# Optimization experiments

Hardware: AMD Instinct MI355X
Metric: run time of the kernel (lower is better)

The kernel has to match this reference:

```python
import jax, jax.numpy as jnp
import numpy as np

B, SEQ_LEN, IN_DIM = 16, 1024, 768
R = 0.1
PI = 3.1415926


def conv1d(x, w, b):
    # x: [B,C,L], w: [O,I,3], 'same' padding, stride 1
    y = jax.lax.conv_general_dilated(x, w, window_strides=(1,), padding=[(1, 1)],
                                     dimension_numbers=('NCH', 'OIH', 'NCH'))
    return y + b[None, :, None]


def layernorm_cl(x, g, b, eps=1e-5):
    # torch nn.LayerNorm((C, L)): normalize jointly over the last two dims of [B,C,L]
    m = x.mean(axis=(1, 2), keepdims=True)
    v = x.var(axis=(1, 2), keepdims=True)
    return (x - m) / jnp.sqrt(v + eps) * g[None] + b[None]


def setup_inputs() -> dict:
    key = jax.random.key(0)
    ks = jax.random.split(key, 8)
    D, D2, L = IN_DIM, IN_DIM * 2, SEQ_LEN
    sc1 = 1.0 / np.sqrt(D * 3)
    sc2 = 1.0 / np.sqrt(D2 * 3)
    return {
        'feats': jax.random.normal(ks[0], (B, L, D), dtype=jnp.float32),
        'conv1_w': jax.random.normal(ks[1], (D2, D, 3), dtype=jnp.float32) * sc1,
        'conv1_b': jnp.zeros((D2,), jnp.float32),
        'ln1_w': jnp.ones((D2, L), jnp.float32),
        'ln1_b': jnp.zeros((D2, L), jnp.float32),
        'conv2_w': jax.random.normal(ks[2], (D2, D2, 3), dtype=jnp.float32) * sc2,
        'conv2_b': jnp.zeros((D2,), jnp.float32),
        'ln2_w': jnp.ones((D2, L), jnp.float32),
        'ln2_b': jnp.zeros((D2, L), jnp.float32),
        'conv3_w': jax.random.normal(ks[3], (2, D2, 3), dtype=jnp.float32) * sc2,
        'conv3_b': jnp.zeros((2,), jnp.float32),
        'ln3_w': jnp.ones((2, L), jnp.float32),
        'ln3_b': jnp.zeros((2, L), jnp.float32),
    }


def reference(feats, conv1_w, conv1_b, ln1_w, ln1_b, conv2_w, conv2_b, ln2_w, ln2_b,
              conv3_w, conv3_b, ln3_w, ln3_b):
    # NOTE: original uses nn.LeakyReLU(True) -> negative_slope=1.0, i.e. identity.
    x = jnp.transpose(feats, (0, 2, 1))                 # [B,D,L]
    h = layernorm_cl(conv1d(x, conv1_w, conv1_b), ln1_w, ln1_b)
    h = layernorm_cl(conv1d(h, conv2_w, conv2_b), ln2_w, ln2_b)
    h = layernorm_cl(conv1d(h, conv3_w, conv3_b), ln3_w, ln3_b)  # [B,2,L]
    s = jax.nn.softmax(h[:, 0, :], axis=1)              # [B,L]
    w = jax.nn.softmax(h[:, 1, :], axis=1)              # [B,L]
    # Vectorized over all centers i: std[b,i] = R*L*s[b,i]
    std = R * SEQ_LEN * s                               # [B,L]
    pos = jnp.arange(SEQ_LEN, dtype=feats.dtype)
    diff2 = (pos[None, :] - pos[:, None]) ** 2          # [i_center, j]
    c = (2.0 * PI) ** -0.5
    gauss = c / std[:, :, None] * jnp.exp(-diff2[None] / (1e-05 + 2.0 * std[:, :, None] ** 2))
    gauss = gauss / jnp.max(gauss, axis=2, keepdims=True)
    att = gauss * w[:, None, :]                         # [B,L_center,L]
    out = jnp.einsum('bij,bjd->bid', att, feats)        # [B,L,D]
    return out
```

## Files before the change

### kernel.cpp

```cpp
#include <hip/hip_runtime.h>
#include <hip/hip_bf16.h>
#include <cstdint>

#define B_   16
#define L_   1024
#define D_   768
#define D2_  1536

typedef __attribute__((ext_vector_type(8))) short bf16x8;
typedef __attribute__((ext_vector_type(4))) float f32x4;

__device__ __forceinline__ float ldin(const void* p, size_t i, int bf) {
  if (bf) return __bfloat162float(((const __hip_bfloat16*)p)[i]);
  return ((const float*)p)[i];
}
__device__ __forceinline__ unsigned short f2bs(float f) {
  __hip_bfloat16 h = __float2bfloat16(f);
  return *(unsigned short*)&h;
}
__device__ __forceinline__ float bs2f(unsigned short u) {
  __hip_bfloat16 h; *(unsigned short*)&h = u;
  return __bfloat162float(h);
}

__device__ __forceinline__ void gload16(const unsigned short* g, unsigned short* l) {
  __builtin_amdgcn_global_load_lds(
      (const __attribute__((address_space(1))) unsigned int*)g,
      (__attribute__((address_space(3))) unsigned int*)l, 16, 0, 0);
}

__global__ void k_detect(const void* __restrict__ ln1w, int* __restrict__ flag) {
  if (threadIdx.x == 0) {
    unsigned u = *(const unsigned*)ln1w;
    *flag = (u == 0x3F800000u) ? 0 : 1;
  }
}

__global__ __launch_bounds__(256) void k_cvt_x(const void* __restrict__ in,
                                               unsigned short* __restrict__ out,
                                               const int* __restrict__ flag) {
  const int bf = *flag;
  const size_t total = (size_t)B_ * (L_ + 2) * D_;
  for (size_t i = (size_t)blockIdx.x * 256 + threadIdx.x; i < total; i += (size_t)gridDim.x * 256) {
    size_t b = i / ((L_ + 2) * D_);
    size_t rem = i - b * (L_ + 2) * D_;
    int pr = (int)(rem / D_);
    int ci = (int)(rem - (size_t)pr * D_);
    float v = 0.f;
    if (pr >= 1 && pr <= L_) v = ldin(in, (b * L_ + pr - 1) * D_ + ci, bf);
    out[i] = f2bs(v);
  }
}

template<int IC>
__global__ __launch_bounds__(256) void k_cvt_w(const void* __restrict__ w,
                                               unsigned short* __restrict__ wp,
                                               const int* __restrict__ flag) {
  const int bf = *flag;
  const int n = D2_ * 3 * IC;
  for (int e = blockIdx.x * 256 + threadIdx.x; e < n; e += gridDim.x * 256) {
    int o = e / (3 * IC); int rem = e - o * 3 * IC;
    int t = rem / IC;     int ci = rem - t * IC;
    wp[e] = f2bs(ldin(w, ((size_t)o * IC + ci) * 3 + t, bf));
  }
}

__global__ __launch_bounds__(256) void k_cvt_lnp(const void* __restrict__ src,
                                                 unsigned short* __restrict__ dst,
                                                 const int* __restrict__ flag) {
  const int bf = *flag;
  __shared__ float t[32][33];
  const int l0 = blockIdx.x * 32, c0 = blockIdx.y * 32;
  const int tx = threadIdx.x, ty = threadIdx.y;
#pragma unroll
  for (int k = 0; k < 4; ++k)
    t[ty + k * 8][tx] = ldin(src, (size_t)(c0 + ty + k * 8) * L_ + l0 + tx, bf);
  __syncthreads();
#pragma unroll
  for (int k = 0; k < 4; ++k)
    dst[(size_t)(l0 + ty + k * 8) * D2_ + c0 + tx] = f2bs(t[tx][ty + k * 8]);
}

__global__ __launch_bounds__(256) void k_zero_hpad(unsigned short* __restrict__ hbp, int G) {
  int i = blockIdx.x * 256 + threadIdx.x;
  int per = 2 * D2_;
  if (i >= G * per) return;
  int lb = i / per; int rem = i - lb * per;
  int w = rem / D2_; int c = rem - w * D2_;
  hbp[((size_t)lb * (L_ + 2) + (size_t)w * (L_ + 1)) * D2_ + c] = 0;
}

template<int IC>
__global__ __launch_bounds__(256, 1) void k_conv_mfma(const unsigned short* __restrict__ x,
                                                      const unsigned short* __restrict__ wp,
                                                      const void* __restrict__ bias,
                                                      unsigned short* __restrict__ hout,
                                                      float* __restrict__ part,
                                                      const int* __restrict__ flag, int b0) {
  __shared__ __attribute__((aligned(16))) unsigned short Xs0[258 * 32];
  __shared__ __attribute__((aligned(16))) unsigned short Xs1[258 * 32];
  __shared__ __attribute__((aligned(16))) unsigned short Ws0[3 * 128 * 32];
  __shared__ __attribute__((aligned(16))) unsigned short Ws1[3 * 128 * 32];
  __shared__ float rs[4], rss[4];
  const int l0 = blockIdx.x * 256, o0 = blockIdx.y * 128, lb = blockIdx.z;
  const int tid = threadIdx.x;
  const int lane = tid & 63, wid = tid >> 6;
  const int wm = wid >> 1, wn = wid & 1;
  const int lr = lane & 15, lg = lane >> 4;

  f32x4 acc[8][4];
#pragma unroll
  for (int m = 0; m < 8; ++m)
#pragma unroll
    for (int n = 0; n < 4; ++n)
      acc[m][n] = (f32x4){0.f, 0.f, 0.f, 0.f};

  const int sx = ((1 + (tid >> 2)) >> 1) & 3;
  const int sw = (tid >> 3) & 3;
  const unsigned short* xbase = x + ((size_t)lb * (L_ + 2) + l0 + 1 + (tid >> 2)) * IC
                                  + (size_t)((tid & 3) ^ sx) * 8;
  const unsigned short* wbase = wp + (size_t)(o0 + (tid >> 2)) * 3 * IC
                                   + (size_t)((tid & 3) ^ sw) * 8;

  auto STAGE = [&](unsigned short* Xd, unsigned short* Wd, int ci0) {
    const unsigned short* xsp = xbase + ci0;
    const unsigned short* wsp = wbase + ci0;
#pragma unroll
    for (int k = 0; k < 4; ++k)
      gload16(xsp + (size_t)k * 64 * IC, Xd + 32 + tid * 8 + k * 2048);
#pragma unroll
    for (int k = 0; k < 6; ++k)
      gload16(wsp + (size_t)((k & 1) * 192 + (k >> 1)) * IC, Wd + tid * 8 + k * 2048);
    if (tid < 8) {
      int r = (tid >> 2) * 257, cs = tid & 3;
      bf16x8 hv = *(const bf16x8*)(x + ((size_t)lb * (L_ + 2) + l0 + r) * IC + ci0 + cs * 8);
      *(bf16x8*)(Xd + r * 32 + cs * 8) = hv;
    }
  };

  auto COMPUTE = [&](const unsigned short* Xd, const unsigned short* Wd) {
    const int pb = (((lr >> 1) & 3) ^ lg) * 8;
#pragma unroll
    for (int t = 0; t < 3; ++t) {
      const int pa = (((((lr + t) >> 1)) & 3) ^ lg) * 8;
      bf16x8 a[8], b[4];
#pragma unroll
      for (int m = 0; m < 8; ++m)
        a[m] = *(const bf16x8*)&Xd[(wm * 128 + m * 16 + lr + t) * 32 + pa];
#pragma unroll
      for (int n = 0; n < 4; ++n)
        b[n] = *(const bf16x8*)&Wd[(t * 128 + wn * 64 + n * 16 + lr) * 32 + pb];
      __builtin_amdgcn_s_setprio(1);
#pragma unroll
      for (int m = 0; m < 8; ++m)
#pragma unroll
        for (int n = 0; n < 4; ++n)
          acc[m][n] = __builtin_amdgcn_mfma_f32_16x16x32_bf16(a[m], b[n], acc[m][n], 0, 0, 0);
      __builtin_amdgcn_s_setprio(0);
    }
  };

  STAGE(Xs0, Ws0, 0);
  asm volatile("s_waitcnt vmcnt(0) lgkmcnt(0)" ::: "memory");
  __builtin_amdgcn_s_barrier();
  for (int ci0 = 0; ci0 < IC; ci0 += 64) {
    if (ci0 + 32 < IC) STAGE(Xs1, Ws1, ci0 + 32);
    COMPUTE(Xs0, Ws0);
    asm volatile("s_waitcnt vmcnt(0) lgkmcnt(0)" ::: "memory");
    __builtin_amdgcn_s_barrier();
    if (ci0 + 64 < IC) STAGE(Xs0, Ws0, ci0 + 64);
    COMPUTE(Xs1, Ws1);
    asm volatile("s_waitcnt vmcnt(0) lgkmcnt(0)" ::: "memory");
    __builtin_amdgcn_s_barrier();
  }

  const int bf = *flag;
  float s = 0.f, ss = 0.f;
  unsigned short* hb = hout + ((size_t)lb * (L_ + 2) + 1) * D2_;
#pragma unroll
  for (int n = 0; n < 4; ++n) {
    int oo = o0 + wn * 64 + n * 16 + lr;
    float bv = ldin(bias, oo, bf);
#pragma unroll
    for (int m = 0; m < 8; ++m) {
      int lbase = l0 + wm * 128 + m * 16 + lg * 4;
#pragma unroll
      for (int j = 0; j < 4; ++j) {
        float v = acc[m][n][j] + bv;
        hb[(size_t)(lbase + j) * D2_ + oo] = f2bs(v);
        s += v; ss += v * v;
      }
    }
  }
#pragma unroll
  for (int o = 32; o > 0; o >>= 1) { s += __shfl_down(s, o); ss += __shfl_down(ss, o); }
  if (lane == 0) { rs[wid] = s; rss[wid] = ss; }
  __syncthreads();
  if (tid == 0) {
    size_t pi = ((size_t)(b0 + lb) * 48 + blockIdx.y * 4 + blockIdx.x) * 2;
    part[pi]     = rs[0] + rs[1] + rs[2] + rs[3];
    part[pi + 1] = rss[0] + rss[1] + rss[2] + rss[3];
  }
}

__global__ void k_stats_final(const float* __restrict__ part, float* __restrict__ stat,
                              int NP, float invN, int b0) {
  const int b = b0 + blockIdx.x;
  float s = 0.f, ss = 0.f;
  for (int p = threadIdx.x; p < NP; p += blockDim.x) {
    s  += part[(size_t)(b * NP + p) * 2];
    ss += part[(size_t)(b * NP + p) * 2 + 1];
  }
#pragma unroll
  for (int o = 32; o > 0; o >>= 1) { s += __shfl_down(s, o); ss += __shfl_down(ss, o); }
  __shared__ float rs[2], rss[2];
  int lane = threadIdx.x & 63, wv = threadIdx.x >> 6;
  if (lane == 0) { rs[wv] = s; rss[wv] = ss; }
  __syncthreads();
  if (threadIdx.x == 0) {
    float m = (rs[0] + rs[1]) * invN;
    float var = (rss[0] + rss[1]) * invN - m * m;
    stat[b * 2] = m;
    stat[b * 2 + 1] = rsqrtf(var + 1e-5f);
  }
}

__global__ __launch_bounds__(256) void k_ln_inplace(unsigned short* __restrict__ hbp,
                                                    const unsigned short* __restrict__ gp,
                                                    const unsigned short* __restrict__ bp,
                                                    const float* __restrict__ stat, int b0) {
  const int lb = blockIdx.y;
  const float m = stat[(b0 + lb) * 2], rstd = stat[(b0 + lb) * 2 + 1];
  const int per8 = D2_ * L_ / 8;
  unsigned short* h = hbp + ((size_t)lb * (L_ + 2) + 1) * D2_;
  for (int e = blockIdx.x * 256 + threadIdx.x; e < per8; e += gridDim.x * 256) {
    bf16x8 v = *(bf16x8*)(h + (size_t)e * 8);
    bf16x8 g = *(const bf16x8*)(gp + (size_t)e * 8);
    bf16x8 bb = *(const bf16x8*)(bp + (size_t)e * 8);
    bf16x8 o;
#pragma unroll
    for (int j = 0; j < 8; ++j)
      o[j] = (short)f2bs((bs2f((unsigned short)v[j]) - m) * rstd * bs2f((unsigned short)g[j])
                         + bs2f((unsigned short)bb[j]));
    *(bf16x8*)(h + (size_t)e * 8) = o;
  }
}

__global__ __launch_bounds__(256) void k_conv3b(const unsigned short* __restrict__ hbp,
                                                const void* __restrict__ w3,
                                                const void* __restrict__ b3,
                                                float* __restrict__ y3,
                                                const int* __restrict__ flag, int b0) {
  __shared__ unsigned short w3s[2 * 3 * D2_];
  const int bf = *flag;
  const int lb = blockIdx.y, gb = b0 + lb;
  const int tid = threadIdx.x, lane = tid & 63, wid = tid >> 6;
  for (int e = tid; e < 2 * 3 * D2_; e += 256) {
    int ch = e / (3 * D2_); int rem = e - ch * 3 * D2_;
    int t = rem / D2_;      int c = rem - t * D2_;
    w3s[e] = f2bs(ldin(w3, ((size_t)ch * D2_ + c) * 3 + t, bf));
  }
  __syncthreads();
  const int l = blockIdx.x * 4 + wid;
  float a0 = 0.f, a1 = 0.f;
#pragma unroll
  for (int t = 0; t < 3; ++t) {
    const unsigned short* hr = hbp + ((size_t)lb * (L_ + 2) + l + t) * D2_;
    const unsigned short* w0 = w3s + t * D2_;
    const unsigned short* w1 = w3s + (3 + t) * D2_;
#pragma unroll
    for (int i = 0; i < 3; ++i) {
      int c0 = (i * 64 + lane) * 8;
      bf16x8 hv  = *(const bf16x8*)(hr + c0);
      bf16x8 wv0 = *(const bf16x8*)(w0 + c0);
      bf16x8 wv1 = *(const bf16x8*)(w1 + c0);
#pragma unroll
      for (int j = 0; j < 8; ++j) {
        float h = bs2f((unsigned short)hv[j]);
        a0 += h * bs2f((unsigned short)wv0[j]);
        a1 += h * bs2f((unsigned short)wv1[j]);
      }
    }
  }
#pragma unroll
  for (int o = 32; o > 0; o >>= 1) { a0 += __shfl_down(a0, o); a1 += __shfl_down(a1, o); }
  if (lane == 0) {
    y3[((size_t)gb * 2) * L_ + l]     = a0 + ldin(b3, 0, bf);
    y3[((size_t)gb * 2 + 1) * L_ + l] = a1 + ldin(b3, 1, bf);
  }
}

__global__ void k_stats3(const float* __restrict__ y3, float* __restrict__ stat3, int b0) {
  const int b = b0 + blockIdx.x;
  const float* p = y3 + (size_t)b * 2 * L_;
  float s = 0.f, ss = 0.f;
  for (int i = threadIdx.x; i < 2 * L_; i += 256) { float v = p[i]; s += v; ss += v * v; }
#pragma unroll
  for (int o = 32; o > 0; o >>= 1) { s += __shfl_down(s, o); ss += __shfl_down(ss, o); }
  __shared__ float rs[4], rss[4];
  int lane = threadIdx.x & 63, wv = threadIdx.x >> 6;
  if (lane == 0) { rs[wv] = s; rss[wv] = ss; }
  __syncthreads();
  if (threadIdx.x == 0) {
    float invN = 1.f / (2 * L_);
    float m = (rs[0] + rs[1] + rs[2] + rs[3]) * invN;
    float var = (rss[0] + rss[1] + rss[2] + rss[3]) * invN - m * m;
    stat3[b * 2] = m;
    stat3[b * 2 + 1] = rsqrtf(var + 1e-5f);
  }
}

__global__ __launch_bounds__(256) void k_softmax(const float* __restrict__ y3,
                                                 const void* __restrict__ g,
                                                 const void* __restrict__ bt,
                                                 const float* __restrict__ stat3,
                                                 float* __restrict__ sw,
                                                 const int* __restrict__ flag, int b0) {
  const int bf = *flag;
  const int ch = blockIdx.x, gb = b0 + blockIdx.y, tid = threadIdx.x;
  const float m = stat3[gb * 2], rstd = stat3[gb * 2 + 1];
  const float* yp = y3 + ((size_t)gb * 2 + ch) * L_;
  float z[4];
  float mx = -1e30f;
#pragma unroll
  for (int k = 0; k < 4; ++k) {
    int l = tid + k * 256;
    z[k] = (yp[l] - m) * rstd * ldin(g, (size_t)ch * L_ + l, bf) + ldin(bt, (size_t)ch * L_ + l, bf);
    mx = fmaxf(mx, z[k]);
  }
#pragma unroll
  for (int o = 32; o > 0; o >>= 1) mx = fmaxf(mx, __shfl_xor(mx, o));
  __shared__ float red[4];
  int lane = tid & 63, wv = tid >> 6;
  if (lane == 0) red[wv] = mx;
  __syncthreads();
  mx = fmaxf(fmaxf(red[0], red[1]), fmaxf(red[2], red[3]));
  float e[4], sum = 0.f;
#pragma unroll
  for (int k = 0; k < 4; ++k) { e[k] = __expf(z[k] - mx); sum += e[k]; }
#pragma unroll
  for (int o = 32; o > 0; o >>= 1) sum += __shfl_xor(sum, o);
  __shared__ float red2[4];
  if (lane == 0) red2[wv] = sum;
  __syncthreads();
  sum = red2[0] + red2[1] + red2[2] + red2[3];
  float inv = 1.f / sum;
#pragma unroll
  for (int k = 0; k < 4; ++k) {
    int l = tid + k * 256;
    sw[((size_t)ch * B_ + gb) * L_ + l] = e[k] * inv;
  }
}

__global__ __launch_bounds__(256) void k_attn(const float* __restrict__ sw,
                                              const void* __restrict__ feats,
                                              void* __restrict__ out,
                                              const int* __restrict__ flag) {
  const int i = blockIdx.x, b = blockIdx.y, tid = threadIdx.x;
  const float s = sw[(size_t)b * L_ + i];
  const float* wv = sw + (size_t)B_ * L_ + (size_t)b * L_;
  const float stdv = 102.4f * s;
  const float denom = 1e-5f + 2.f * stdv * stdv;
  const float inv = 1.f / denom;
  int r = (int)ceilf(sqrtf(30.f * denom));
  int jlo = i - r; if (jlo < 0) jlo = 0;
  int jhi = i + r; if (jhi > L_ - 1) jhi = L_ - 1;
  float a0 = 0.f, a1 = 0.f, a2 = 0.f;
  const int bf = *flag;
  if (bf) {
    const __hip_bfloat16* fb = (const __hip_bfloat16*)feats + (size_t)b * L_ * D_ + tid;
    for (int j = jlo; j <= jhi; ++j) {
      float d = (float)(j - i);
      float gz = __expf(-d * d * inv) * wv[j];
      const __hip_bfloat16* f = fb + (size_t)j * D_;
      a0 += gz * __bfloat162float(f[0]);
      a1 += gz * __bfloat162float(f[256]);
      a2 += gz * __bfloat162float(f[512]);
    }
    __hip_bfloat16* op = (__hip_bfloat16*)out + ((size_t)b * L_ + i) * D_ + tid;
    op[0]   = __float2bfloat16(a0);
    op[256] = __float2bfloat16(a1);
    op[512] = __float2bfloat16(a2);
  } else {
    const float* fb = (const float*)feats + (size_t)b * L_ * D_ + tid;
    for (int j = jlo; j <= jhi; ++j) {
      float d = (float)(j - i);
      float gz = __expf(-d * d * inv) * wv[j];
      const float* f = fb + (size_t)j * D_;
      a0 += gz * f[0];
      a1 += gz * f[256];
      a2 += gz * f[512];
    }
    float* op = (float*)out + ((size_t)b * L_ + i) * D_ + tid;
    op[0] = a0; op[256] = a1; op[512] = a2;
  }
}

extern "C" void kernel_launch(void* const* d_in, const int* in_sizes, int n_in,
                              void* d_out, int out_size, void* d_ws, size_t ws_size,
                              hipStream_t stream) {
  (void)in_sizes; (void)n_in; (void)out_size;
  char* wsb = (char*)d_ws;
  size_t off = 0;
  auto alloc = [&](size_t bytes) -> char* {
    char* p = wsb + off;
    off += (bytes + 255) & ~(size_t)255;
    return p;
  };
  unsigned short* xbp  = (unsigned short*)alloc((size_t)B_ * (L_ + 2) * D_ * 2);
  unsigned short* wp1  = (unsigned short*)alloc((size_t)D2_ * 3 * D_ * 2);
  unsigned short* wp2  = (unsigned short*)alloc((size_t)D2_ * 3 * D2_ * 2);
  unsigned short* lp1w = (unsigned short*)alloc((size_t)D2_ * L_ * 2);
  unsigned short* lp1b = (unsigned short*)alloc((size_t)D2_ * L_ * 2);
  unsigned short* lp2w = (unsigned short*)alloc((size_t)D2_ * L_ * 2);
  unsigned short* lp2b = (unsigned short*)alloc((size_t)D2_ * L_ * 2);
  float* y3   = (float*)alloc((size_t)B_ * 2 * L_ * 4);
  float* swb  = (float*)alloc((size_t)2 * B_ * L_ * 4);
  float* part = (float*)alloc((size_t)B_ * 48 * 2 * 4);
  float* stat = (float*)alloc((size_t)B_ * 2 * 4);
  float* st3  = (float*)alloc((size_t)B_ * 2 * 4);
  int*   flag = (int*)alloc(16);
  const size_t fixed = off;

  int G = 1;
  const int cand[5] = {16, 8, 4, 2, 1};
  for (int k = 0; k < 5; ++k) {
    size_t need = fixed + (size_t)cand[k] * (size_t)(L_ + 2) * D2_ * 2 * 2 + 1024;
    if (need <= ws_size) { G = cand[k]; break; }
  }
  unsigned short* Hbp1 = (unsigned short*)alloc((size_t)G * (L_ + 2) * D2_ * 2);
  unsigned short* Hbp2 = (unsigned short*)alloc((size_t)G * (L_ + 2) * D2_ * 2);

  k_detect<<<1, 64, 0, stream>>>(d_in[3], flag);

  k_cvt_x<<<2048, 256, 0, stream>>>(d_in[0], xbp, flag);
  k_cvt_w<768><<<2048, 256, 0, stream>>>(d_in[1], wp1, flag);
  k_cvt_w<1536><<<2048, 256, 0, stream>>>(d_in[5], wp2, flag);
  dim3 tg(32, 48), tb(32, 8);
  k_cvt_lnp<<<tg, tb, 0, stream>>>(d_in[3], lp1w, flag);
  k_cvt_lnp<<<tg, tb, 0, stream>>>(d_in[4], lp1b, flag);
  k_cvt_lnp<<<tg, tb, 0, stream>>>(d_in[7], lp2w, flag);
  k_cvt_lnp<<<tg, tb, 0, stream>>>(d_in[8], lp2b, flag);
  k_zero_hpad<<<(G * 2 * D2_ + 255) / 256, 256, 0, stream>>>(Hbp1, G);
  k_zero_hpad<<<(G * 2 * D2_ + 255) / 256, 256, 0, stream>>>(Hbp2, G);

  const float invN = 1.f / (float)(D2_ * L_);
  for (int b0 = 0; b0 < B_; b0 += G) {
    k_conv_mfma<768><<<dim3(4, 12, G), 256, 0, stream>>>(
        xbp + (size_t)b0 * (L_ + 2) * D_, wp1, d_in[2], Hbp1, part, flag, b0);
    k_stats_final<<<G, 128, 0, stream>>>(part, stat, 48, invN, b0);
    k_ln_inplace<<<dim3(768, G), 256, 0, stream>>>(Hbp1, lp1w, lp1b, stat, b0);

    k_conv_mfma<1536><<<dim3(4, 12, G), 256, 0, stream>>>(
        Hbp1, wp2, d_in[6], Hbp2, part, flag, b0);
    k_stats_final<<<G, 128, 0, stream>>>(part, stat, 48, invN, b0);
    k_ln_inplace<<<dim3(768, G), 256, 0, stream>>>(Hbp2, lp2w, lp2b, stat, b0);

    k_conv3b<<<dim3(L_ / 4, G), 256, 0, stream>>>(Hbp2, d_in[9], d_in[10], y3, flag, b0);
    k_stats3<<<G, 256, 0, stream>>>(y3, st3, b0);
    k_softmax<<<dim3(2, G), 256, 0, stream>>>(y3, d_in[11], d_in[12], st3, swb, flag, b0);
  }

  k_attn<<<dim3(L_, B_), 256, 0, stream>>>(swb, d_in[0], d_out, flag);
}
```

Measured before the change: 594.6 us.

## Single-buffer conv weight tile in LDS to fit two blocks per CU

The conv MFMA kernel drops the double-buffered weight tile in LDS and keeps only the input tile double-buffered. Weights for the next step are loaded after a barrier that follows compute, so they are no longer overlapped with the MFMAs. The halo rows are staged through registers. Launch bounds move from 1 to 2 blocks per CU, which cuts LDS per block so two blocks can be resident and hide latency, at the cost of an extra barrier per step and exposed weight-load latency.

```diff
diff --git a/kernel.cpp b/kernel.cpp
--- a/kernel.cpp
+++ b/kernel.cpp
@@ -43,7 +43,7 @@
   const size_t total = (size_t)B_ * (L_ + 2) * D_;
   for (size_t i = (size_t)blockIdx.x * 256 + threadIdx.x; i < total; i += (size_t)gridDim.x * 256) {
     size_t b = i / ((L_ + 2) * D_);
-    size_t rem = i - b * (L_ + 2) * D_;
+    size_t rem = i - b * ((size_t)(L_ + 2) * D_);
     int pr = (int)(rem / D_);
     int ci = (int)(rem - (size_t)pr * D_);
     float v = 0.f;
@@ -91,7 +91,7 @@
 }
 
 template<int IC>
-__global__ __launch_bounds__(256, 1) void k_conv_mfma(const unsigned short* __restrict__ x,
+__global__ __launch_bounds__(256, 2) void k_conv_mfma(const unsigned short* __restrict__ x,
                                                       const unsigned short* __restrict__ wp,
                                                       const void* __restrict__ bias,
                                                       unsigned short* __restrict__ hout,
@@ -99,8 +99,7 @@
                                                       const int* __restrict__ flag, int b0) {
   __shared__ __attribute__((aligned(16))) unsigned short Xs0[258 * 32];
   __shared__ __attribute__((aligned(16))) unsigned short Xs1[258 * 32];
-  __shared__ __attribute__((aligned(16))) unsigned short Ws0[3 * 128 * 32];
-  __shared__ __attribute__((aligned(16))) unsigned short Ws1[3 * 128 * 32];
+  __shared__ __attribute__((aligned(16))) unsigned short Ws[3 * 128 * 32];
   __shared__ float rs[4], rss[4];
   const int l0 = blockIdx.x * 256, o0 = blockIdx.y * 128, lb = blockIdx.z;
   const int tid = threadIdx.x;
@@ -121,35 +120,31 @@
                                   + (size_t)((tid & 3) ^ sx) * 8;
   const unsigned short* wbase = wp + (size_t)(o0 + (tid >> 2)) * 3 * IC
                                    + (size_t)((tid & 3) ^ sw) * 8;
-
-  auto STAGE = [&](unsigned short* Xd, unsigned short* Wd, int ci0) {
-    const unsigned short* xsp = xbase + ci0;
-    const unsigned short* wsp = wbase + ci0;
+  const int hr = (tid >> 2) * 257, hcs = tid & 3;
+  const unsigned short* hbase = x + ((size_t)lb * (L_ + 2) + l0 + hr) * IC + hcs * 8;
+
+  auto STAGE_X = [&](unsigned short* Xd, int ci) {
 #pragma unroll
     for (int k = 0; k < 4; ++k)
-      gload16(xsp + (size_t)k * 64 * IC, Xd + 32 + tid * 8 + k * 2048);
+      gload16(xbase + ci + (size_t)k * 64 * IC, Xd + 32 + tid * 8 + k * 2048);
+  };
+  auto STAGE_W = [&](int ci) {
 #pragma unroll
     for (int k = 0; k < 6; ++k)
-      gload16(wsp + (size_t)((k & 1) * 192 + (k >> 1)) * IC, Wd + tid * 8 + k * 2048);
-    if (tid < 8) {
-      int r = (tid >> 2) * 257, cs = tid & 3;
-      bf16x8 hv = *(const bf16x8*)(x + ((size_t)lb * (L_ + 2) + l0 + r) * IC + ci0 + cs * 8);
-      *(bf16x8*)(Xd + r * 32 + cs * 8) = hv;
-    }
+      gload16(wbase + ci + (size_t)((k & 1) * 192 + (k >> 1)) * IC, Ws + tid * 8 + k * 2048);
   };
-
-  auto COMPUTE = [&](const unsigned short* Xd, const unsigned short* Wd) {
+  auto COMPUTE = [&](const unsigned short* Xd) {
     const int pb = (((lr >> 1) & 3) ^ lg) * 8;
 #pragma unroll
     for (int t = 0; t < 3; ++t) {
-      const int pa = (((((lr + t) >> 1)) & 3) ^ lg) * 8;
+      const int pa = ((((lr + t) >> 1) & 3) ^ lg) * 8;
       bf16x8 a[8], b[4];
 #pragma unroll
       for (int m = 0; m < 8; ++m)
         a[m] = *(const bf16x8*)&Xd[(wm * 128 + m * 16 + lr + t) * 32 + pa];
 #pragma unroll
       for (int n = 0; n < 4; ++n)
-        b[n] = *(const bf16x8*)&Wd[(t * 128 + wn * 64 + n * 16 + lr) * 32 + pb];
+        b[n] = *(const bf16x8*)&Ws[(t * 128 + wn * 64 + n * 16 + lr) * 32 + pb];
       __builtin_amdgcn_s_setprio(1);
 #pragma unroll
       for (int m = 0; m < 8; ++m)
@@ -160,18 +155,46 @@
     }
   };
 
-  STAGE(Xs0, Ws0, 0);
+  bf16x8 hreg = {0, 0, 0, 0, 0, 0, 0, 0};
+  if (tid < 8) hreg = *(const bf16x8*)(hbase + 0);
+  STAGE_X(Xs0, 0);
+  STAGE_W(0);
+  if (tid < 8) *(bf16x8*)(Xs0 + hr * 32 + hcs * 8) = hreg;
   asm volatile("s_waitcnt vmcnt(0) lgkmcnt(0)" ::: "memory");
   __builtin_amdgcn_s_barrier();
+
   for (int ci0 = 0; ci0 < IC; ci0 += 64) {
-    if (ci0 + 32 < IC) STAGE(Xs1, Ws1, ci0 + 32);
-    COMPUTE(Xs0, Ws0);
-    asm volatile("s_waitcnt vmcnt(0) lgkmcnt(0)" ::: "memory");
-    __builtin_amdgcn_s_barrier();
-    if (ci0 + 64 < IC) STAGE(Xs0, Ws0, ci0 + 64);
-    COMPUTE(Xs1, Ws1);
-    asm volatile("s_waitcnt vmcnt(0) lgkmcnt(0)" ::: "memory");
-    __builtin_amdgcn_s_barrier();
+    {
+      const int cin = ci0 + 32;
+      if (tid < 8) hreg = *(const bf16x8*)(hbase + cin);
+      STAGE_X(Xs1, cin);
+      COMPUTE(Xs0);
+      __builtin_amdgcn_sched_barrier(0);
+      __builtin_amdgcn_s_barrier();
+      __builtin_amdgcn_sched_barrier(0);
+      STAGE_W(cin);
+      if (tid < 8) *(bf16x8*)(Xs1 + hr * 32 + hcs * 8) = hreg;
+      asm volatile("s_waitcnt vmcnt(0) lgkmcnt(0)" ::: "memory");
+      __builtin_amdgcn_s_barrier();
+    }
+    {
+      const int cin = ci0 + 64;
+      const bool more = cin < IC;
+      if (more) {
+        if (tid < 8) hreg = *(const bf16x8*)(hbase + cin);
+        STAGE_X(Xs0, cin);
+      }
+      COMPUTE(Xs1);
+      if (more) {
+        __builtin_amdgcn_sched_barrier(0);
+        __builtin_amdgcn_s_barrier();
+        __builtin_amdgcn_sched_barrier(0);
+        STAGE_W(cin);
+        if (tid < 8) *(bf16x8*)(Xs0 + hr * 32 + hcs * 8) = hreg;
+        asm volatile("s_waitcnt vmcnt(0) lgkmcnt(0)" ::: "memory");
+        __builtin_amdgcn_s_barrier();
+      }
+    }
   }
 
   const int bf = *flag;
```

Result: faster. 505.5 us (-15.0%).
